# Optimization experiments

Measured on AMD Instinct MI355X. Metric: run time of the kernel, lower is better.

The kernel has to match this reference:

```python
import jax, jax.numpy as jnp
import numpy as np

C, G, S, L, B = 16, 8192, 8, 3, 32


def setup_inputs() -> dict:
    key = jax.random.key(0)
    kx, kI = jax.random.split(key)
    # x: valuation vector over G ground atoms per batch element, in [0,1)
    x = jax.random.uniform(kx, (B, G), dtype=jnp.float32)
    # I: precomputed index tensor [C, G, S, L], indices into the G axis of x
    I = jax.random.randint(kI, (C, G, S, L), 0, G, dtype=jnp.int64)
    return {"x": x, "I": I}


def reference(x, I):
    # Equivalent of: for each clause i, gather(V_tild, 1, I_i) -> prod over L -> sum over S
    # torch gather semantics: out[b, g, s, l] = x[b, I[i, g, s, l]]
    # Vectorized over all clauses at once; no repeat/broadcast materialization beyond the gather.
    gathered = x[:, I]                        # [B, C, G, S, L]
    body = jnp.prod(gathered, axis=-1)        # conjunction over L body literals -> [B, C, G, S]
    clause_val = jnp.sum(body, axis=-1)       # sum over S substitutions -> [B, C, G]
    # torch.stack over clauses puts C first: [C, B, G]
    return jnp.transpose(clause_val, (1, 0, 2))
```

## Files before the change

kernel.cpp:

```cpp
#include <hip/hip_runtime.h>
#include <stdint.h>

#define Cc 16
#define Gg 8192
#define Ss 8
#define Ll 3
#define Bb 32

#define ZS 4
#define THREADS 512

__device__ __forceinline__ void async_load16(const void* gsrc, void* lds) {
    uint32_t l32 = (uint32_t)__builtin_amdgcn_readfirstlane((uint32_t)(uintptr_t)lds);
    __builtin_amdgcn_global_load_lds(
        (const __attribute__((address_space(1))) uint32_t*)(uintptr_t)gsrc,
        (__attribute__((address_space(3))) uint32_t*)(uintptr_t)l32,
        16, 0, 0);
}

__device__ __forceinline__ uint32_t f2bf(float f) {
    uint32_t u = __float_as_uint(f);
    return (u + 0x7fffu + ((u >> 16) & 1u)) >> 16;
}

__global__ __launch_bounds__(256) void pack_idx(const int* __restrict__ I,
                                                ushort* __restrict__ I16) {
    int t = blockIdx.x * 256 + threadIdx.x;
    int4 v = ((const int4*)I)[t];
    ushort4 o = { (ushort)v.x, (ushort)v.y, (ushort)v.z, (ushort)v.w };
    ((ushort4*)I16)[t] = o;
}

__global__ __launch_bounds__(256) void build_xh(const float* __restrict__ x,
                                                uint4* __restrict__ xh) {
    int t = blockIdx.x * 256 + threadIdx.x;
    int z = t >> 13;
    int g = t & (Gg - 1);
    uint32_t w[4];
    #pragma unroll
    for (int j = 0; j < 4; ++j) {
        uint32_t lo = f2bf(x[(size_t)(8 * z + 2 * j) * Gg + g]);
        uint32_t hi = f2bf(x[(size_t)(8 * z + 2 * j + 1) * Gg + g]);
        w[j] = lo | (hi << 16);
    }
    xh[t] = make_uint4(w[0], w[1], w[2], w[3]);
}

__global__ __launch_bounds__(THREADS) void clause_bf16(const uint4* __restrict__ xh,
                                                       const ushort* __restrict__ I16,
                                                       float* __restrict__ out) {
    __shared__ uint4 xl[Gg];
    const int tid = threadIdx.x;
    const int z = blockIdx.y;
    const int flat = blockIdx.x * THREADS + tid;
    const int c = flat >> 13;
    const int g = flat & (Gg - 1);

    {
        const char* gs = (const char*)(xh + (size_t)z * Gg);
        char* ls = (char*)xl;
        const int lane = tid & 63;
        const int w = tid >> 6;
        #pragma unroll
        for (int i = 0; i < 16; ++i) {
            int off = ((w << 4) | i) << 10;
            async_load16(gs + off + lane * 16, ls + off);
        }
    }

    const uint4* ip = (const uint4*)(I16 + (size_t)(c * Gg + g) * (Ss * Ll));
    uint4 i0 = ip[0], i1 = ip[1], i2 = ip[2];

    __syncthreads();

    uint32_t wd[12] = {i0.x, i0.y, i0.z, i0.w, i1.x, i1.y, i1.z, i1.w,
                       i2.x, i2.y, i2.z, i2.w};
    uint4 v[Ss * Ll];
    #pragma unroll
    for (int k = 0; k < Ss * Ll; ++k) {
        uint32_t idx = (k & 1) ? (wd[k >> 1] >> 16) : (wd[k >> 1] & 0xffffu);
        v[k] = xl[idx];
    }

    float acc[8] = {0.f, 0.f, 0.f, 0.f, 0.f, 0.f, 0.f, 0.f};
    #pragma unroll
    for (int s = 0; s < Ss; ++s) {
        const uint4 a = v[3 * s], b = v[3 * s + 1], d = v[3 * s + 2];
        const uint32_t* ua = &a.x;
        const uint32_t* ub = &b.x;
        const uint32_t* ud = &d.x;
        #pragma unroll
        for (int j = 0; j < 4; ++j) {
            float a0 = __uint_as_float(ua[j] << 16);
            float a1 = __uint_as_float(ua[j] & 0xffff0000u);
            float b0 = __uint_as_float(ub[j] << 16);
            float b1 = __uint_as_float(ub[j] & 0xffff0000u);
            float d0 = __uint_as_float(ud[j] << 16);
            float d1 = __uint_as_float(ud[j] & 0xffff0000u);
            acc[2 * j]     += a0 * b0 * d0;
            acc[2 * j + 1] += a1 * b1 * d1;
        }
    }

    float* op = out + ((size_t)(c * Bb + z * 8)) * Gg + g;
    #pragma unroll
    for (int j = 0; j < 8; ++j)
        op[(size_t)j * Gg] = acc[j];
}

__global__ __launch_bounds__(256) void clause_kernel_direct(const float* __restrict__ x,
                                                            const int* __restrict__ I,
                                                            float* __restrict__ out) {
    const int tid = threadIdx.x;
    const int b = tid & 31;
    const int j = tid >> 5;
    const int g = blockIdx.x * 8 + j;
    const int c = blockIdx.y;

    const int* Icg = I + (size_t)(c * Gg + g) * (Ss * Ll);
    float sum = 0.f;
    #pragma unroll
    for (int s = 0; s < Ss; ++s) {
        float p0 = x[(size_t)b * Gg + Icg[3 * s + 0]];
        float p1 = x[(size_t)b * Gg + Icg[3 * s + 1]];
        float p2 = x[(size_t)b * Gg + Icg[3 * s + 2]];
        sum += p0 * p1 * p2;
    }
    out[(size_t)(c * Bb + b) * Gg + g] = sum;
}

extern "C" void kernel_launch(void* const* d_in, const int* in_sizes, int n_in,
                              void* d_out, int out_size, void* d_ws, size_t ws_size,
                              hipStream_t stream) {
    const float* x = (const float*)d_in[0];
    const int* I = (const int*)d_in[1];
    float* out = (float*)d_out;

    const size_t nIdx = (size_t)Cc * Gg * Ss * Ll;
    const size_t xh_bytes = (size_t)ZS * Gg * sizeof(uint4);
    const size_t i16_bytes = nIdx * sizeof(ushort);

    if (ws_size >= xh_bytes + i16_bytes) {
        uint4* xh = (uint4*)d_ws;
        ushort* I16 = (ushort*)((char*)d_ws + xh_bytes);
        pack_idx<<<(int)(nIdx / 4 / 256), 256, 0, stream>>>(I, I16);
        build_xh<<<(ZS * Gg) / 256, 256, 0, stream>>>(x, xh);
        clause_bf16<<<dim3((Cc * Gg) / THREADS, ZS), THREADS, 0, stream>>>(xh, I16, out);
    } else {
        clause_kernel_direct<<<dim3(Gg / 8, Cc), 256, 0, stream>>>(x, I, out);
    }
}
```

Before: 89.77 us.

## Switch gathered table to fp16 with packed half2 multiplies and two items per thread

Stores the packed x table as fp16 instead of bf16 and computes each triple product with packed half2 multiplies, converting to fp32 only for the sum. Each block now handles two tiles of 512 g values, so the 128KB LDS fill is amortised over twice the work and half as many blocks are launched. fp16 has more mantissa bits than bf16, but the products are computed in half precision, and halving the block count lowers parallelism.

New measurement: 84.55 us. 5.8% less time.

```diff
diff --git a/kernel.cpp b/kernel.cpp
--- a/kernel.cpp
+++ b/kernel.cpp
@@ -1,4 +1,5 @@
 #include <hip/hip_runtime.h>
+#include <hip/hip_fp16.h>
 #include <stdint.h>
 
 #define Cc 16
@@ -9,6 +10,7 @@
 
 #define ZS 4
 #define THREADS 512
+#define ITERS 2
 
 __device__ __forceinline__ void async_load16(const void* gsrc, void* lds) {
     uint32_t l32 = (uint32_t)__builtin_amdgcn_readfirstlane((uint32_t)(uintptr_t)lds);
@@ -16,11 +18,6 @@
         (const __attribute__((address_space(1))) uint32_t*)(uintptr_t)gsrc,
         (__attribute__((address_space(3))) uint32_t*)(uintptr_t)l32,
         16, 0, 0);
-}
-
-__device__ __forceinline__ uint32_t f2bf(float f) {
-    uint32_t u = __float_as_uint(f);
-    return (u + 0x7fffu + ((u >> 16) & 1u)) >> 16;
 }
 
 __global__ __launch_bounds__(256) void pack_idx(const int* __restrict__ I,
@@ -39,22 +36,21 @@
     uint32_t w[4];
     #pragma unroll
     for (int j = 0; j < 4; ++j) {
-        uint32_t lo = f2bf(x[(size_t)(8 * z + 2 * j) * Gg + g]);
-        uint32_t hi = f2bf(x[(size_t)(8 * z + 2 * j + 1) * Gg + g]);
-        w[j] = lo | (hi << 16);
+        __half2 h = __floats2half2_rn(x[(size_t)(8 * z + 2 * j) * Gg + g],
+                                      x[(size_t)(8 * z + 2 * j + 1) * Gg + g]);
+        w[j] = *(const uint32_t*)&h;
     }
     xh[t] = make_uint4(w[0], w[1], w[2], w[3]);
 }
 
-__global__ __launch_bounds__(THREADS) void clause_bf16(const uint4* __restrict__ xh,
-                                                       const ushort* __restrict__ I16,
-                                                       float* __restrict__ out) {
+__global__ __launch_bounds__(THREADS) void clause_f16(const uint4* __restrict__ xh,
+                                                      const ushort* __restrict__ I16,
+                                                      float* __restrict__ out) {
     __shared__ uint4 xl[Gg];
     const int tid = threadIdx.x;
     const int z = blockIdx.y;
-    const int flat = blockIdx.x * THREADS + tid;
-    const int c = flat >> 13;
-    const int g = flat & (Gg - 1);
+    const int c = blockIdx.x >> 3;
+    const int gbase = (blockIdx.x & 7) * (THREADS * ITERS);
 
     {
         const char* gs = (const char*)(xh + (size_t)z * Gg);
@@ -68,44 +64,50 @@
         }
     }
 
-    const uint4* ip = (const uint4*)(I16 + (size_t)(c * Gg + g) * (Ss * Ll));
-    uint4 i0 = ip[0], i1 = ip[1], i2 = ip[2];
+    uint4 iq[ITERS][3];
+    #pragma unroll
+    for (int it = 0; it < ITERS; ++it) {
+        int g = gbase + it * THREADS + tid;
+        const uint4* ip = (const uint4*)(I16 + ((size_t)c * Gg + g) * (Ss * Ll));
+        iq[it][0] = ip[0]; iq[it][1] = ip[1]; iq[it][2] = ip[2];
+    }
 
     __syncthreads();
 
-    uint32_t wd[12] = {i0.x, i0.y, i0.z, i0.w, i1.x, i1.y, i1.z, i1.w,
-                       i2.x, i2.y, i2.z, i2.w};
-    uint4 v[Ss * Ll];
     #pragma unroll
-    for (int k = 0; k < Ss * Ll; ++k) {
-        uint32_t idx = (k & 1) ? (wd[k >> 1] >> 16) : (wd[k >> 1] & 0xffffu);
-        v[k] = xl[idx];
+    for (int it = 0; it < ITERS; ++it) {
+        const int g = gbase + it * THREADS + tid;
+        uint32_t wd[12] = {iq[it][0].x, iq[it][0].y, iq[it][0].z, iq[it][0].w,
+                           iq[it][1].x, iq[it][1].y, iq[it][1].z, iq[it][1].w,
+                           iq[it][2].x, iq[it][2].y, iq[it][2].z, iq[it][2].w};
+
+        uint4 v[Ss * Ll];
+        #pragma unroll
+        for (int k = 0; k < Ss * Ll; ++k) {
+            uint32_t idx = (k & 1) ? (wd[k >> 1] >> 16) : (wd[k >> 1] & 0xffffu);
+            v[k] = xl[idx];
+        }
+
+        float acc[8] = {0.f, 0.f, 0.f, 0.f, 0.f, 0.f, 0.f, 0.f};
+        #pragma unroll
+        for (int s = 0; s < Ss; ++s) {
+            const __half2* a = (const __half2*)&v[3 * s];
+            const __half2* b = (const __half2*)&v[3 * s + 1];
+            const __half2* d = (const __half2*)&v[3 * s + 2];
+            #pragma unroll
+            for (int j = 0; j < 4; ++j) {
+                __half2 p = __hmul2(__hmul2(a[j], b[j]), d[j]);
+                float2 pf = __half22float2(p);
+                acc[2 * j]     += pf.x;
+                acc[2 * j + 1] += pf.y;
+            }
+        }
+
+        float* op = out + ((size_t)(c * Bb + 8 * z)) * Gg + g;
+        #pragma unroll
+        for (int j = 0; j < 8; ++j)
+            op[(size_t)j * Gg] = acc[j];
     }
-
-    float acc[8] = {0.f, 0.f, 0.f, 0.f, 0.f, 0.f, 0.f, 0.f};
-    #pragma unroll
-    for (int s = 0; s < Ss; ++s) {
-        const uint4 a = v[3 * s], b = v[3 * s + 1], d = v[3 * s + 2];
-        const uint32_t* ua = &a.x;
-        const uint32_t* ub = &b.x;
-        const uint32_t* ud = &d.x;
-        #pragma unroll
-        for (int j = 0; j < 4; ++j) {
-            float a0 = __uint_as_float(ua[j] << 16);
-            float a1 = __uint_as_float(ua[j] & 0xffff0000u);
-            float b0 = __uint_as_float(ub[j] << 16);
-            float b1 = __uint_as_float(ub[j] & 0xffff0000u);
-            float d0 = __uint_as_float(ud[j] << 16);
-            float d1 = __uint_as_float(ud[j] & 0xffff0000u);
-            acc[2 * j]     += a0 * b0 * d0;
-            acc[2 * j + 1] += a1 * b1 * d1;
-        }
-    }
-
-    float* op = out + ((size_t)(c * Bb + z * 8)) * Gg + g;
-    #pragma unroll
-    for (int j = 0; j < 8; ++j)
-        op[(size_t)j * Gg] = acc[j];
 }
 
 __global__ __launch_bounds__(256) void clause_kernel_direct(const float* __restrict__ x,
@@ -145,7 +147,7 @@
         ushort* I16 = (ushort*)((char*)d_ws + xh_bytes);
         pack_idx<<<(int)(nIdx / 4 / 256), 256, 0, stream>>>(I, I16);
         build_xh<<<(ZS * Gg) / 256, 256, 0, stream>>>(x, xh);
-        clause_bf16<<<dim3((Cc * Gg) / THREADS, ZS), THREADS, 0, stream>>>(xh, I16, out);
+        clause_f16<<<dim3((Cc * Gg) / (THREADS * ITERS), ZS), THREADS, 0, stream>>>(xh, I16, out);
     } else {
         clause_kernel_direct<<<dim3(Gg / 8, Cc), 256, 0, stream>>>(x, I, out);
     }
```
